# Performance work log

Measured on AMD Instinct MI355X. Metric: run time of the kernel, lower is better.

Reference implementation:

```python
import jax, jax.numpy as jnp
import numpy as np

N_NODES = 50000
N_EDGES = 800000
C = 128
NEG_SLOPE = 0.01  # nn.LeakyReLU default


def _init_linear(key, fan_in, fan_out):
    kw, kb = jax.random.split(key)
    lim = 1.0 / np.sqrt(fan_in)
    W = jax.random.uniform(kw, (fan_in, fan_out), jnp.float32, -lim, lim)
    b = jax.random.uniform(kb, (fan_out,), jnp.float32, -lim, lim)
    return W, b


def setup_inputs() -> dict:
    key = jax.random.key(0)
    ks = jax.random.split(key, 10)
    x = jax.random.normal(ks[0], (N_NODES, C), jnp.float32)
    pos = jax.random.normal(ks[1], (N_NODES, 3), jnp.float32)
    edge_index = jax.random.randint(ks[2], (2, N_EDGES), 0, N_NODES, jnp.int64)
    # mlp_h: Linear(C,C) -> LeakyReLU -> Linear(C,3) -> Tanh
    Wh1, bh1 = _init_linear(ks[3], C, C)
    Wh2, bh2 = _init_linear(ks[4], C, 3)
    # mlp_f: Linear(C+3, C) -> LeakyReLU
    Wf, bf = _init_linear(ks[5], C + 3, C)
    # mlp_g: Linear(C,C) -> LeakyReLU -> Linear(C,C)
    Wg1, bg1 = _init_linear(ks[6], C, C)
    Wg2, bg2 = _init_linear(ks[7], C, C)
    return {"x": x, "pos": pos, "edge_index": edge_index,
            "Wh1": Wh1, "bh1": bh1, "Wh2": Wh2, "bh2": bh2,
            "Wf": Wf, "bf": bf,
            "Wg1": Wg1, "bg1": bg1, "Wg2": Wg2, "bg2": bg2}


def reference(x, pos, edge_index, Wh1, bh1, Wh2, bh2, Wf, bf, Wg1, bg1, Wg2, bg2):
    lrelu = lambda t: jax.nn.leaky_relu(t, NEG_SLOPE)
    # delta_i = tanh(mlp_h(x_i))  -> [N, 3]
    delta = jnp.tanh(lrelu(x @ Wh1 + bh1) @ Wh2 + bh2)
    src, dst = edge_index[0], edge_index[1]  # message j -> i (PyG convention)
    # per-edge relative position: pos_j - pos_i + delta_i  -> [E, 3]
    rel = pos[src] - pos[dst] + delta[dst]
    # per-edge message: mlp_f([rel, x_j])  -> [E, C]
    e = lrelu(jnp.concatenate([rel, x[src]], axis=-1) @ Wf + bf)
    # scatter-max aggregate over incoming edges per target node
    agg = jax.ops.segment_max(e, dst, num_segments=N_NODES)
    agg = jnp.where(jnp.isfinite(agg), agg, 0.0)  # empty segments -> 0
    # out_i = mlp_g(agg_i) + x_i
    out = lrelu(agg @ Wg1 + bg1) @ Wg2 + bg2 + x
    return out
```

## Files before the change

kernel.cpp:

```cpp
#include <hip/hip_runtime.h>
#include <cfloat>
#include <cmath>

#define NEG_SLOPE 0.01f

typedef __attribute__((ext_vector_type(8))) short short8;
typedef __attribute__((ext_vector_type(4))) float f32x4;

__device__ __forceinline__ float lrelu(float v) { return v >= 0.0f ? v : NEG_SLOPE * v; }

__device__ __forceinline__ ushort f2b(float f) {
    unsigned u = __float_as_uint(f);
    u += 0x7fffu + ((u >> 16) & 1u);
    return (ushort)(u >> 16);
}
__device__ __forceinline__ float b2f(ushort s) { return __uint_as_float(((unsigned)s) << 16); }

__device__ __forceinline__ void split8(const float* v, short8& hi, short8& lo) {
#pragma unroll
    for (int j = 0; j < 8; ++j) {
        ushort h = f2b(v[j]);
        hi[j] = (short)h;
        lo[j] = (short)f2b(v[j] - b2f(h));
    }
}

__global__ __launch_bounds__(256) void count_wprep_kernel(
    const int* __restrict__ ei,
    const float* __restrict__ Wh1, const float* __restrict__ Wf,
    const float* __restrict__ Wg1, const float* __restrict__ Wg2,
    ushort* __restrict__ WT, int* __restrict__ G, int E, int NBK)
{
    __shared__ int cnt[256];
    const int t = threadIdx.x;
    const int b = blockIdx.x;

    {
        int tt = b * 256 + t;
        int mat = tt >> 14;
        int idx = tt & 16383;
        int n = idx >> 7, k = idx & 127;
        float v;
        if (mat == 0)      v = Wh1[k * 128 + n];
        else if (mat == 1) v = Wf[(k + 3) * 128 + n];
        else if (mat == 2) v = Wg1[k * 128 + n];
        else               v = Wg2[k * 128 + n];
        WT[(tt - idx) + n * 128 + k] = f2b(v);
    }

    cnt[t] = 0;
    __syncthreads();
    for (int e = b * 256 + t; e < E; e += 65536)
        atomicAdd(&cnt[ei[E + e] >> 8], 1);
    __syncthreads();
    if (t < NBK) G[t * 256 + b] = cnt[t];
}

__global__ __launch_bounds__(256) void scanA_kernel(
    const int* __restrict__ G, int* __restrict__ partial)
{
    __shared__ int s[256];
    int i = blockIdx.x * 256 + threadIdx.x;
    s[threadIdx.x] = G[i];
    __syncthreads();
    for (int d = 128; d > 0; d >>= 1) {
        if (threadIdx.x < d) s[threadIdx.x] += s[threadIdx.x + d];
        __syncthreads();
    }
    if (threadIdx.x == 0) partial[blockIdx.x] = s[0];
}

__global__ __launch_bounds__(256) void scanBC_kernel(
    int* __restrict__ G, const int* __restrict__ partial, int NB)
{
    __shared__ int s[256];
    __shared__ int base;
    const int t = threadIdx.x;
    int v = (t < NB) ? partial[t] : 0;
    s[t] = v;
    __syncthreads();
    for (int d = 1; d < 256; d <<= 1) {
        int a = (t >= d) ? s[t - d] : 0;
        __syncthreads();
        s[t] += a;
        __syncthreads();
    }
    if (t == blockIdx.x) base = s[t] - v;
    __syncthreads();

    int i = blockIdx.x * 256 + t;
    int g = G[i];
    s[t] = g;
    __syncthreads();
    for (int d = 1; d < 256; d <<= 1) {
        int a = (t >= d) ? s[t - d] : 0;
        __syncthreads();
        s[t] += a;
        __syncthreads();
    }
    G[i] = base + s[t] - g;
}

__global__ __launch_bounds__(256) void partition_kernel(
    const int* __restrict__ ei, const int* __restrict__ G,
    uint* __restrict__ bpairs, int E, int NBK)
{
    __shared__ int cur[256];
    const int tid = threadIdx.x;
    if (tid < NBK) cur[tid] = G[tid * 256 + blockIdx.x];
    __syncthreads();
    for (int e = blockIdx.x * 256 + tid; e < E; e += 65536) {
        int src = ei[e];
        int dst = ei[E + e];
        int p = atomicAdd(&cur[dst >> 8], 1);
        bpairs[p] = (uint)src | ((uint)(dst & 255) << 24);
    }
}

__global__ __launch_bounds__(256) void bucket_csr_kernel(
    const uint* __restrict__ bpairs, const int* __restrict__ G,
    int* __restrict__ offs, int* __restrict__ srcs, int E, int M, int NBK)
{
    __shared__ int deg[256], scn[256], cur[256];
    const int b = blockIdx.x;
    const int t = threadIdx.x;
    const int base = G[b * 256];
    const int end  = (b + 1 < NBK) ? G[(b + 1) * 256] : E;
    deg[t] = 0;
    __syncthreads();
    for (int p = base + t; p < end; p += 256)
        atomicAdd(&deg[bpairs[p] >> 24], 1);
    __syncthreads();
    scn[t] = deg[t];
    __syncthreads();
    for (int d = 1; d < 256; d <<= 1) {
        int a = (t >= d) ? scn[t - d] : 0;
        __syncthreads();
        scn[t] += a;
        __syncthreads();
    }
    int excl = scn[t] - deg[t];
    cur[t] = excl;
    int node = b * 256 + t;
    if (node < M) offs[node] = base + excl;
    if (node == M - 1 || (b == NBK - 1 && t == 255)) offs[M] = E;
    __syncthreads();
    for (int p = base + t; p < end; p += 256) {
        uint pk = bpairs[p];
        int qpos = atomicAdd(&cur[pk >> 24], 1);
        srcs[base + qpos] = (int)(pk & 0xFFFFFFu);
    }
}


#define GEMM_CORE_REG(ACC, AH, AL)                                              \
    {                                                                           \
        _Pragma("unroll")                                                       \
        for (int ks = 0; ks < 4; ++ks) {                                        \
            _Pragma("unroll")                                                   \
            for (int nt = 0; nt < 8; ++nt) {                                    \
                short8 bfr = *(const short8*)&Bs[(nt * 16 + ln) * 136 + ks * 32 + qd * 8]; \
                ACC[nt] = __builtin_amdgcn_mfma_f32_16x16x32_bf16(AL[ks], bfr, ACC[nt], 0, 0, 0); \
                ACC[nt] = __builtin_amdgcn_mfma_f32_16x16x32_bf16(AH[ks], bfr, ACC[nt], 0, 0, 0); \
            }                                                                   \
        }                                                                       \
    }

#define STAGE_B(WTP)                                                            \
    {                                                                           \
        _Pragma("unroll")                                                       \
        for (int i = 0; i < 8; ++i) {                                           \
            int c = tid + 256 * i;                                              \
            int r = c >> 4, col8 = (c & 15) * 8;                                \
            *(uint4*)&Bs[r * 136 + col8] = *(const uint4*)((WTP) + r * 128 + col8); \
        }                                                                       \
    }

__global__ __launch_bounds__(256) void hy_kernel(
    const float* __restrict__ x, const ushort* __restrict__ Wh1T,
    const float* __restrict__ bh1, const float* __restrict__ Wh2,
    const float* __restrict__ bh2, const ushort* __restrict__ WfxT,
    const float* __restrict__ Wf, const float* __restrict__ pos,
    float* __restrict__ q, ushort* __restrict__ yb, int M)
{
    __shared__ ushort Bs[128 * 136];
    __shared__ ushort yS[64 * 128];
    const int tid = threadIdx.x;
    const int w = tid >> 6, L = tid & 63, qd = L >> 4, ln = L & 15;
    const int row0 = blockIdx.x * 64;
    const int arow = row0 + w * 16 + ln;

    short8 ah[4], al[4];
    {
        const float* base = x + (size_t)((arow < M) ? arow : 0) * 128 + qd * 8;
        float vb[8];
#pragma unroll
        for (int ks = 0; ks < 4; ++ks) {
            float4 v0 = make_float4(0.f, 0.f, 0.f, 0.f), v1 = v0;
            if (arow < M) {
                v0 = *(const float4*)(base + ks * 32);
                v1 = *(const float4*)(base + ks * 32 + 4);
            }
            vb[0] = v0.x; vb[1] = v0.y; vb[2] = v0.z; vb[3] = v0.w;
            vb[4] = v1.x; vb[5] = v1.y; vb[6] = v1.z; vb[7] = v1.w;
            split8(vb, ah[ks], al[ks]);
        }
    }

    STAGE_B(Wh1T);
    __syncthreads();
    f32x4 acc1[8];
#pragma unroll
    for (int nt = 0; nt < 8; ++nt) acc1[nt] = (f32x4){0.f, 0.f, 0.f, 0.f};
    GEMM_CORE_REG(acc1, ah, al);
    __syncthreads();

    STAGE_B(WfxT);
    __syncthreads();
    f32x4 acc2[8];
#pragma unroll
    for (int nt = 0; nt < 8; ++nt) acc2[nt] = (f32x4){0.f, 0.f, 0.f, 0.f};
    GEMM_CORE_REG(acc2, ah, al);
    __syncthreads();

    float* h1s = (float*)Bs;
#pragma unroll
    for (int nt = 0; nt < 8; ++nt) {
        int n = nt * 16 + ln;
        float bias = bh1[n];
#pragma unroll
        for (int r = 0; r < 4; ++r)
            h1s[(w * 16 + qd * 4 + r) * 132 + n] = lrelu(acc1[nt][r] + bias);
    }
#pragma unroll
    for (int r = 0; r < 4; ++r) {
        int m = w * 16 + qd * 4 + r;
        int gm = row0 + m;
        float p0 = 0.f, p1 = 0.f, p2 = 0.f;
        if (gm < M) { p0 = pos[gm * 3]; p1 = pos[gm * 3 + 1]; p2 = pos[gm * 3 + 2]; }
#pragma unroll
        for (int nt = 0; nt < 8; ++nt) {
            int n = nt * 16 + ln;
            yS[m * 128 + n] = f2b(acc2[nt][r] + p0 * Wf[n] + p1 * Wf[128 + n] + p2 * Wf[256 + n]);
        }
    }
    __syncthreads();

    int row = tid & 63, cc = tid >> 6;
    if (cc < 3 && row0 + row < M) {
        float s = 0.f;
#pragma unroll
        for (int k4 = 0; k4 < 32; ++k4) {
            float4 h = *(const float4*)&h1s[row * 132 + k4 * 4];
            s += h.x * Wh2[(k4 * 4 + 0) * 3 + cc] + h.y * Wh2[(k4 * 4 + 1) * 3 + cc]
               + h.z * Wh2[(k4 * 4 + 2) * 3 + cc] + h.w * Wh2[(k4 * 4 + 3) * 3 + cc];
        }
        q[(row0 + row) * 3 + cc] = tanhf(s + bh2[cc]) - pos[(row0 + row) * 3 + cc];
    }
#pragma unroll
    for (int i = 0; i < 4; ++i) {
        int c = tid + 256 * i;
        int r = c >> 4, col8 = (c & 15) * 8;
        if (row0 + r < M)
            *(uint4*)(yb + (size_t)(row0 + r) * 128 + col8) = *(const uint4*)&yS[r * 128 + col8];
    }
}

__global__ __launch_bounds__(256) void midout_kernel(
    const ushort* __restrict__ aggb, const float* __restrict__ qv,
    const float* __restrict__ Wf, const float* __restrict__ bfv,
    const ushort* __restrict__ Wg1T, const float* __restrict__ bg1,
    const ushort* __restrict__ Wg2T, const float* __restrict__ bg2,
    const float* __restrict__ x, float* __restrict__ out, int M)
{
    __shared__ ushort Bs[128 * 136];
    __shared__ ushort Ms[64 * 136];
    const int tid = threadIdx.x;
    const int w = tid >> 6, L = tid & 63, qd = L >> 4, ln = L & 15;
    const int row0 = blockIdx.x * 64;
    const int arow = row0 + w * 16 + ln;

    short8 ah[4], al[4];
    {
        bool ok = arow < M;
        const ushort* base = aggb + (size_t)(ok ? arow : 0) * 128 + qd * 8;
        float q0 = 0.f, q1 = 0.f, q2 = 0.f;
        if (ok) { q0 = qv[arow * 3]; q1 = qv[arow * 3 + 1]; q2 = qv[arow * 3 + 2]; }
        float vb[8];
#pragma unroll
        for (int ks = 0; ks < 4; ++ks) {
            union { uint4 u; ushort s[8]; } a;
            a.u = ok ? *(const uint4*)(base + ks * 32) : make_uint4(0xFF80FF80u, 0xFF80FF80u, 0xFF80FF80u, 0xFF80FF80u);
#pragma unroll
            for (int j = 0; j < 8; ++j) {
                int k = ks * 32 + qd * 8 + j;
                float dec = 0.f;
                if (a.s[j] != 0xFF80u)
                    dec = lrelu(b2f(a.s[j]) + q0 * Wf[k] + q1 * Wf[128 + k] + q2 * Wf[256 + k] + bfv[k]);
                vb[j] = dec;
            }
            split8(vb, ah[ks], al[ks]);
        }
    }

    STAGE_B(Wg1T);
    __syncthreads();
    f32x4 macc[8];
#pragma unroll
    for (int nt = 0; nt < 8; ++nt) macc[nt] = (f32x4){0.f, 0.f, 0.f, 0.f};
    GEMM_CORE_REG(macc, ah, al);
    __syncthreads();

#pragma unroll
    for (int nt = 0; nt < 8; ++nt) {
        int n = nt * 16 + ln;
        float bias = bg1[n];
#pragma unroll
        for (int r = 0; r < 4; ++r)
            Ms[(w * 16 + qd * 4 + r) * 136 + n] = f2b(lrelu(macc[nt][r] + bias));
    }
    STAGE_B(Wg2T);
    __syncthreads();

    short8 a2[4];
#pragma unroll
    for (int ks = 0; ks < 4; ++ks)
        a2[ks] = *(const short8*)&Ms[(w * 16 + ln) * 136 + ks * 32 + qd * 8];

    f32x4 acc2[8];
#pragma unroll
    for (int nt = 0; nt < 8; ++nt) acc2[nt] = (f32x4){0.f, 0.f, 0.f, 0.f};
#pragma unroll
    for (int ks = 0; ks < 4; ++ks) {
#pragma unroll
        for (int nt = 0; nt < 8; ++nt) {
            short8 bfr = *(const short8*)&Bs[(nt * 16 + ln) * 136 + ks * 32 + qd * 8];
            acc2[nt] = __builtin_amdgcn_mfma_f32_16x16x32_bf16(a2[ks], bfr, acc2[nt], 0, 0, 0);
        }
    }
    __syncthreads();

    float* outS = (float*)Bs;
#pragma unroll
    for (int r = 0; r < 4; ++r) {
        int m = w * 16 + qd * 4 + r;
#pragma unroll
        for (int nt = 0; nt < 8; ++nt)
            outS[m * 132 + nt * 16 + ln] = acc2[nt][r];
    }
    __syncthreads();
#pragma unroll
    for (int i = 0; i < 8; ++i) {
        int c = tid + 256 * i;
        int r = c >> 5, col4 = (c & 31) * 4;
        int gr = row0 + r;
        if (gr < M) {
            float4 o = *(const float4*)&outS[r * 132 + col4];
            float4 bv = *(const float4*)(bg2 + col4);
            float4 xv = *(const float4*)(x + (size_t)gr * 128 + col4);
            o.x += bv.x + xv.x; o.y += bv.y + xv.y;
            o.z += bv.z + xv.z; o.w += bv.w + xv.w;
            *(float4*)(out + (size_t)gr * 128 + col4) = o;
        }
    }
}

__global__ __launch_bounds__(256) void agg_kernel(
    const int* __restrict__ offs, const int* __restrict__ srcs,
    const ushort* __restrict__ yb, ushort* __restrict__ aggb, int M)
{
    int wave = threadIdx.x >> 6;
    int lane = threadIdx.x & 63;
    int node = blockIdx.x * 4 + wave;
    if (node >= M) return;
    int o0 = offs[node], o1 = offs[node + 1];
    float a0 = -INFINITY, a1 = -INFINITY;
    const uint* yp = (const uint*)yb;
    int j = o0;
    for (; j + 3 < o1; j += 4) {
        int s0 = srcs[j], s1 = srcs[j + 1], s2 = srcs[j + 2], s3 = srcs[j + 3];
        uint u0 = yp[(size_t)s0 * 64 + lane];
        uint u1 = yp[(size_t)s1 * 64 + lane];
        uint u2 = yp[(size_t)s2 * 64 + lane];
        uint u3 = yp[(size_t)s3 * 64 + lane];
        a0 = fmaxf(a0, fmaxf(fmaxf(__uint_as_float(u0 << 16), __uint_as_float(u1 << 16)),
                             fmaxf(__uint_as_float(u2 << 16), __uint_as_float(u3 << 16))));
        a1 = fmaxf(a1, fmaxf(fmaxf(__uint_as_float(u0 & 0xFFFF0000u), __uint_as_float(u1 & 0xFFFF0000u)),
                             fmaxf(__uint_as_float(u2 & 0xFFFF0000u), __uint_as_float(u3 & 0xFFFF0000u))));
    }
    for (; j < o1; ++j) {
        uint u = yp[(size_t)srcs[j] * 64 + lane];
        a0 = fmaxf(a0, __uint_as_float(u << 16));
        a1 = fmaxf(a1, __uint_as_float(u & 0xFFFF0000u));
    }
    uint pk = (__float_as_uint(a0) >> 16) | (__float_as_uint(a1) & 0xFFFF0000u);
    ((uint*)aggb)[(size_t)node * 64 + lane] = pk;
}

extern "C" void kernel_launch(void* const* d_in, const int* in_sizes, int n_in,
                              void* d_out, int out_size, void* d_ws, size_t ws_size,
                              hipStream_t stream)
{
    const float* x   = (const float*)d_in[0];
    const float* pos = (const float*)d_in[1];
    const int*   ei  = (const int*)d_in[2];
    const float* Wh1 = (const float*)d_in[3];
    const float* bh1 = (const float*)d_in[4];
    const float* Wh2 = (const float*)d_in[5];
    const float* bh2 = (const float*)d_in[6];
    const float* Wf  = (const float*)d_in[7];
    const float* bf  = (const float*)d_in[8];
    const float* Wg1 = (const float*)d_in[9];
    const float* bg1 = (const float*)d_in[10];
    const float* Wg2 = (const float*)d_in[11];
    const float* bg2 = (const float*)d_in[12];
    float* out = (float*)d_out;

    const int M = in_sizes[0] / 128;
    const int E = in_sizes[2] / 2;
    const int NBK = (M + 255) >> 8;

    char* ws = (char*)d_ws;
    size_t off = 0;
    auto alloc = [&](size_t bytes) { void* p = ws + off; off += (bytes + 255) & ~255ull; return p; };
    ushort* yb     = (ushort*)alloc((size_t)M * 128 * sizeof(ushort));
    ushort* aggb   = (ushort*)alloc((size_t)M * 128 * sizeof(ushort));
    ushort* WT     = (ushort*)alloc(4 * 16384 * sizeof(ushort));
    float*  q      = (float*)alloc((size_t)M * 3 * sizeof(float));
    int*    offs   = (int*)alloc((size_t)(M + 1) * sizeof(int));
    int*    G      = (int*)alloc((size_t)NBK * 256 * sizeof(int));
    int*    part   = (int*)alloc(256 * sizeof(int));
    uint*   bpairs = (uint*)alloc((size_t)E * sizeof(uint));
    int*    srcs   = (int*)alloc((size_t)E * sizeof(int));

    const int gb = (M + 63) / 64;

    count_wprep_kernel<<<256, 256, 0, stream>>>(ei, Wh1, Wf, Wg1, Wg2, WT, G, E, NBK);
    scanA_kernel<<<NBK, 256, 0, stream>>>(G, part);
    scanBC_kernel<<<NBK, 256, 0, stream>>>(G, part, NBK);
    partition_kernel<<<256, 256, 0, stream>>>(ei, G, bpairs, E, NBK);
    bucket_csr_kernel<<<NBK, 256, 0, stream>>>(bpairs, G, offs, srcs, E, M, NBK);

    hy_kernel<<<gb, 256, 0, stream>>>(x, WT, bh1, Wh2, bh2,
                                      WT + 16384, Wf, pos, q, yb, M);
    agg_kernel<<<(M + 3) / 4, 256, 0, stream>>>(offs, srcs, yb, aggb, M);
    midout_kernel<<<gb, 256, 0, stream>>>(aggb, q, Wf, bf,
                                          WT + 2 * 16384, bg1,
                                          WT + 3 * 16384, bg2, x, out, M);
}
```

Baseline: 219.1 us.

## Fuse edge counting with node GEMM kernel and fold aggregation into output MLP

Merges the edge-count/weight-prep kernel and the per-node hy GEMM into one launch: the first 256 blocks count edges, the rest compute h/y, with hy staging its weights directly from fp32 global memory (transposed and converted per block). The scatter-max aggregation is moved into midout_kernel, which gathers neighbor rows into shared memory before the Wg1/Wg2 GEMMs, removing the agg kernel, the aggb buffer round-trip and two launches. The cost is strided uncoalesced weight loads in every hy block and a serialized per-wave aggregation loop (16 nodes per wave) inside midout, which may hurt load balance and latency hiding.

```diff
diff --git a/kernel.cpp b/kernel.cpp
--- a/kernel.cpp
+++ b/kernel.cpp
@@ -23,37 +23,6 @@
         hi[j] = (short)h;
         lo[j] = (short)f2b(v[j] - b2f(h));
     }
-}
-
-__global__ __launch_bounds__(256) void count_wprep_kernel(
-    const int* __restrict__ ei,
-    const float* __restrict__ Wh1, const float* __restrict__ Wf,
-    const float* __restrict__ Wg1, const float* __restrict__ Wg2,
-    ushort* __restrict__ WT, int* __restrict__ G, int E, int NBK)
-{
-    __shared__ int cnt[256];
-    const int t = threadIdx.x;
-    const int b = blockIdx.x;
-
-    {
-        int tt = b * 256 + t;
-        int mat = tt >> 14;
-        int idx = tt & 16383;
-        int n = idx >> 7, k = idx & 127;
-        float v;
-        if (mat == 0)      v = Wh1[k * 128 + n];
-        else if (mat == 1) v = Wf[(k + 3) * 128 + n];
-        else if (mat == 2) v = Wg1[k * 128 + n];
-        else               v = Wg2[k * 128 + n];
-        WT[(tt - idx) + n * 128 + k] = f2b(v);
-    }
-
-    cnt[t] = 0;
-    __syncthreads();
-    for (int e = b * 256 + t; e < E; e += 65536)
-        atomicAdd(&cnt[ei[E + e] >> 8], 1);
-    __syncthreads();
-    if (t < NBK) G[t * 256 + b] = cnt[t];
 }
 
 __global__ __launch_bounds__(256) void scanA_kernel(
@@ -176,18 +145,57 @@
         }                                                                       \
     }
 
-__global__ __launch_bounds__(256) void hy_kernel(
-    const float* __restrict__ x, const ushort* __restrict__ Wh1T,
+#define STAGE_B_TF32(WP)                                                        \
+    {                                                                           \
+        _Pragma("unroll")                                                       \
+        for (int i = 0; i < 8; ++i) {                                           \
+            int c = tid + 256 * i;                                              \
+            int n = c >> 4, k8 = (c & 15) * 8;                                  \
+            union { uint4 u; ushort s[8]; } tb;                                 \
+            _Pragma("unroll")                                                   \
+            for (int j = 0; j < 8; ++j) tb.s[j] = f2b((WP)[(k8 + j) * 128 + n]);\
+            *(uint4*)&Bs[n * 136 + k8] = tb.u;                                  \
+        }                                                                       \
+    }
+
+__global__ __launch_bounds__(256) void fused_count_hy_kernel(
+    const int* __restrict__ ei,
+    const float* __restrict__ Wg1, const float* __restrict__ Wg2,
+    ushort* __restrict__ WT, int* __restrict__ G, int E, int NBK,
+    const float* __restrict__ x, const float* __restrict__ Wh1,
     const float* __restrict__ bh1, const float* __restrict__ Wh2,
-    const float* __restrict__ bh2, const ushort* __restrict__ WfxT,
-    const float* __restrict__ Wf, const float* __restrict__ pos,
-    float* __restrict__ q, ushort* __restrict__ yb, int M)
+    const float* __restrict__ bh2, const float* __restrict__ Wf,
+    const float* __restrict__ pos, float* __restrict__ q,
+    ushort* __restrict__ yb, int M)
 {
     __shared__ ushort Bs[128 * 136];
     __shared__ ushort yS[64 * 128];
     const int tid = threadIdx.x;
+
+    if (blockIdx.x < 256) {
+        int* cnt = (int*)yS;
+        const int b = blockIdx.x;
+        {
+            int tt = b * 256 + tid;
+            if (tt < 32768) {
+                int mat = tt >> 14;
+                int idx = tt & 16383;
+                int n = idx >> 7, k = idx & 127;
+                float v = mat ? Wg2[k * 128 + n] : Wg1[k * 128 + n];
+                WT[(tt - idx) + n * 128 + k] = f2b(v);
+            }
+        }
+        cnt[tid] = 0;
+        __syncthreads();
+        for (int e = b * 256 + tid; e < E; e += 65536)
+            atomicAdd(&cnt[ei[E + e] >> 8], 1);
+        __syncthreads();
+        if (tid < NBK) G[tid * 256 + b] = cnt[tid];
+        return;
+    }
+
     const int w = tid >> 6, L = tid & 63, qd = L >> 4, ln = L & 15;
-    const int row0 = blockIdx.x * 64;
+    const int row0 = (blockIdx.x - 256) * 64;
     const int arow = row0 + w * 16 + ln;
 
     short8 ah[4], al[4];
@@ -207,7 +215,7 @@
         }
     }
 
-    STAGE_B(Wh1T);
+    STAGE_B_TF32(Wh1);
     __syncthreads();
     f32x4 acc1[8];
 #pragma unroll
@@ -215,7 +223,7 @@
     GEMM_CORE_REG(acc1, ah, al);
     __syncthreads();
 
-    STAGE_B(WfxT);
+    STAGE_B_TF32(Wf + 3 * 128);
     __syncthreads();
     f32x4 acc2[8];
 #pragma unroll
@@ -267,7 +275,8 @@
 }
 
 __global__ __launch_bounds__(256) void midout_kernel(
-    const ushort* __restrict__ aggb, const float* __restrict__ qv,
+    const int* __restrict__ offs, const int* __restrict__ srcs,
+    const ushort* __restrict__ yb, const float* __restrict__ qv,
     const float* __restrict__ Wf, const float* __restrict__ bfv,
     const ushort* __restrict__ Wg1T, const float* __restrict__ bg1,
     const ushort* __restrict__ Wg2T, const float* __restrict__ bg2,
@@ -278,19 +287,51 @@
     const int tid = threadIdx.x;
     const int w = tid >> 6, L = tid & 63, qd = L >> 4, ln = L & 15;
     const int row0 = blockIdx.x * 64;
-    const int arow = row0 + w * 16 + ln;
+
+    uint* aggS = (uint*)Bs;
+    {
+        const uint* yp = (const uint*)yb;
+        for (int i = 0; i < 16; ++i) {
+            int m = w * 16 + i;
+            int node = row0 + m;
+            float a0 = -INFINITY, a1 = -INFINITY;
+            if (node < M) {
+                int o0 = offs[node], o1 = offs[node + 1];
+                int j = o0;
+                for (; j + 3 < o1; j += 4) {
+                    int s0 = srcs[j], s1 = srcs[j + 1], s2 = srcs[j + 2], s3 = srcs[j + 3];
+                    uint u0 = yp[(size_t)s0 * 64 + L];
+                    uint u1 = yp[(size_t)s1 * 64 + L];
+                    uint u2 = yp[(size_t)s2 * 64 + L];
+                    uint u3 = yp[(size_t)s3 * 64 + L];
+                    a0 = fmaxf(a0, fmaxf(fmaxf(__uint_as_float(u0 << 16), __uint_as_float(u1 << 16)),
+                                         fmaxf(__uint_as_float(u2 << 16), __uint_as_float(u3 << 16))));
+                    a1 = fmaxf(a1, fmaxf(fmaxf(__uint_as_float(u0 & 0xFFFF0000u), __uint_as_float(u1 & 0xFFFF0000u)),
+                                         fmaxf(__uint_as_float(u2 & 0xFFFF0000u), __uint_as_float(u3 & 0xFFFF0000u))));
+                }
+                for (; j < o1; ++j) {
+                    uint u = yp[(size_t)srcs[j] * 64 + L];
+                    a0 = fmaxf(a0, __uint_as_float(u << 16));
+                    a1 = fmaxf(a1, __uint_as_float(u & 0xFFFF0000u));
+                }
+            }
+            aggS[m * 68 + L] = (__float_as_uint(a0) >> 16) | (__float_as_uint(a1) & 0xFFFF0000u);
+        }
+    }
+    __syncthreads();
 
     short8 ah[4], al[4];
     {
+        int mm = w * 16 + ln;
+        int arow = row0 + mm;
         bool ok = arow < M;
-        const ushort* base = aggb + (size_t)(ok ? arow : 0) * 128 + qd * 8;
         float q0 = 0.f, q1 = 0.f, q2 = 0.f;
         if (ok) { q0 = qv[arow * 3]; q1 = qv[arow * 3 + 1]; q2 = qv[arow * 3 + 2]; }
         float vb[8];
 #pragma unroll
         for (int ks = 0; ks < 4; ++ks) {
             union { uint4 u; ushort s[8]; } a;
-            a.u = ok ? *(const uint4*)(base + ks * 32) : make_uint4(0xFF80FF80u, 0xFF80FF80u, 0xFF80FF80u, 0xFF80FF80u);
+            a.u = *(const uint4*)&aggS[mm * 68 + ks * 16 + qd * 4];
 #pragma unroll
             for (int j = 0; j < 8; ++j) {
                 int k = ks * 32 + qd * 8 + j;
@@ -302,6 +343,7 @@
             split8(vb, ah[ks], al[ks]);
         }
     }
+    __syncthreads();
 
     STAGE_B(Wg1T);
     __syncthreads();
@@ -363,38 +405,6 @@
             *(float4*)(out + (size_t)gr * 128 + col4) = o;
         }
     }
-}
-
-__global__ __launch_bounds__(256) void agg_kernel(
-    const int* __restrict__ offs, const int* __restrict__ srcs,
-    const ushort* __restrict__ yb, ushort* __restrict__ aggb, int M)
-{
-    int wave = threadIdx.x >> 6;
-    int lane = threadIdx.x & 63;
-    int node = blockIdx.x * 4 + wave;
-    if (node >= M) return;
-    int o0 = offs[node], o1 = offs[node + 1];
-    float a0 = -INFINITY, a1 = -INFINITY;
-    const uint* yp = (const uint*)yb;
-    int j = o0;
-    for (; j + 3 < o1; j += 4) {
-        int s0 = srcs[j], s1 = srcs[j + 1], s2 = srcs[j + 2], s3 = srcs[j + 3];
-        uint u0 = yp[(size_t)s0 * 64 + lane];
-        uint u1 = yp[(size_t)s1 * 64 + lane];
-        uint u2 = yp[(size_t)s2 * 64 + lane];
-        uint u3 = yp[(size_t)s3 * 64 + lane];
-        a0 = fmaxf(a0, fmaxf(fmaxf(__uint_as_float(u0 << 16), __uint_as_float(u1 << 16)),
-                             fmaxf(__uint_as_float(u2 << 16), __uint_as_float(u3 << 16))));
-        a1 = fmaxf(a1, fmaxf(fmaxf(__uint_as_float(u0 & 0xFFFF0000u), __uint_as_float(u1 & 0xFFFF0000u)),
-                             fmaxf(__uint_as_float(u2 & 0xFFFF0000u), __uint_as_float(u3 & 0xFFFF0000u))));
-    }
-    for (; j < o1; ++j) {
-        uint u = yp[(size_t)srcs[j] * 64 + lane];
-        a0 = fmaxf(a0, __uint_as_float(u << 16));
-        a1 = fmaxf(a1, __uint_as_float(u & 0xFFFF0000u));
-    }
-    uint pk = (__float_as_uint(a0) >> 16) | (__float_as_uint(a1) & 0xFFFF0000u);
-    ((uint*)aggb)[(size_t)node * 64 + lane] = pk;
 }
 
 extern "C" void kernel_launch(void* const* d_in, const int* in_sizes, int n_in,
@@ -424,8 +434,7 @@
     size_t off = 0;
     auto alloc = [&](size_t bytes) { void* p = ws + off; off += (bytes + 255) & ~255ull; return p; };
     ushort* yb     = (ushort*)alloc((size_t)M * 128 * sizeof(ushort));
-    ushort* aggb   = (ushort*)alloc((size_t)M * 128 * sizeof(ushort));
-    ushort* WT     = (ushort*)alloc(4 * 16384 * sizeof(ushort));
+    ushort* WT     = (ushort*)alloc(2 * 16384 * sizeof(ushort));
     float*  q      = (float*)alloc((size_t)M * 3 * sizeof(float));
     int*    offs   = (int*)alloc((size_t)(M + 1) * sizeof(int));
     int*    G      = (int*)alloc((size_t)NBK * 256 * sizeof(int));
@@ -435,16 +444,13 @@
 
     const int gb = (M + 63) / 64;
 
-    count_wprep_kernel<<<256, 256, 0, stream>>>(ei, Wh1, Wf, Wg1, Wg2, WT, G, E, NBK);
+    fused_count_hy_kernel<<<256 + gb, 256, 0, stream>>>(
+        ei, Wg1, Wg2, WT, G, E, NBK,
+        x, Wh1, bh1, Wh2, bh2, Wf, pos, q, yb, M);
     scanA_kernel<<<NBK, 256, 0, stream>>>(G, part);
     scanBC_kernel<<<NBK, 256, 0, stream>>>(G, part, NBK);
     partition_kernel<<<256, 256, 0, stream>>>(ei, G, bpairs, E, NBK);
     bucket_csr_kernel<<<NBK, 256, 0, stream>>>(bpairs, G, offs, srcs, E, M, NBK);
-
-    hy_kernel<<<gb, 256, 0, stream>>>(x, WT, bh1, Wh2, bh2,
-                                      WT + 16384, Wf, pos, q, yb, M);
-    agg_kernel<<<(M + 3) / 4, 256, 0, stream>>>(offs, srcs, yb, aggb, M);
-    midout_kernel<<<gb, 256, 0, stream>>>(aggb, q, Wf, bf,
-                                          WT + 2 * 16384, bg1,
-                                          WT + 3 * 16384, bg2, x, out, M);
-}
+    midout_kernel<<<gb, 256, 0, stream>>>(offs, srcs, yb, q, Wf, bf,
+                                          WT, bg1, WT + 16384, bg2, x, out, M);
+}
```

New measurement: 330.8 us. 1.51x slower.
